# Optimization experiments

Hardware: AMD Instinct MI355X
Metric: run time of the kernel (lower is better)

## Reference

```python
import jax, jax.numpy as jnp
import numpy as np

N = 262144   # occupied voxels
H = 64       # channels
G = 128      # dense grid extent per axis (coords in [0, G))
K = 27       # 3x3x3 kernel offsets


def _build_neighbor_map():
    rng = np.random.default_rng(0)
    lin = rng.choice(G ** 3, size=N, replace=False).astype(np.int64)
    coords = np.stack(np.unravel_index(lin, (G, G, G)), axis=1)  # [N,3]
    table = np.full(G ** 3, N, dtype=np.int32)  # sentinel N -> zero row
    table[lin] = np.arange(N, dtype=np.int32)
    offs = np.array([(dx, dy, dz) for dx in (-1, 0, 1)
                     for dy in (-1, 0, 1) for dz in (-1, 0, 1)], dtype=np.int64)
    nbr = np.full((N, K), N, dtype=np.int32)
    for k in range(K):
        nc = coords + offs[k]
        ok = np.all((nc >= 0) & (nc < G), axis=1)
        nl = nc[ok, 0] * G * G + nc[ok, 1] * G + nc[ok, 2]
        nbr[ok, k] = table[nl]
    return nbr


def setup_inputs() -> dict:
    key = jax.random.key(0)
    k1, k2, k3 = jax.random.split(key, 3)
    scale = 1.0 / np.sqrt(K * H)  # ME-style fan-in init scale
    x = jax.random.normal(k1, (N, H), dtype=jnp.float32)
    Wa = jax.random.normal(k2, (K, H, H), dtype=jnp.float32) * scale
    Wb = jax.random.normal(k3, (K, H, H), dtype=jnp.float32) * scale
    nbr = jnp.asarray(_build_neighbor_map())
    return {"x": x, "Wa": Wa, "Wb": Wb, "nbr": nbr}


def _sparse_conv(feats, W, nbr):
    # gather -> GEMM -> accumulate, per kernel offset (missing neighbors hit zero row)
    fpad = jnp.concatenate([feats, jnp.zeros((1, feats.shape[1]), feats.dtype)], axis=0)
    out = jnp.zeros((feats.shape[0], W.shape[2]), feats.dtype)
    for k in range(W.shape[0]):
        out = out + fpad[nbr[:, k]] @ W[k]
    return out


def reference(x, Wa, Wb, nbr):
    out = _sparse_conv(x, Wa, nbr)          # spconva
    out = jax.nn.relu(out)                  # MinkowskiReLU
    out = _sparse_conv(out, Wb, nbr)        # spconvb
    return out + x                          # residual add
```

## Files before the change

### kernel.cpp

```cpp
#include <hip/hip_runtime.h>


#define N_ROWS 262144
#define HCH    64
#define KOFF   27
#define CHUNK  3

typedef unsigned short u16;
typedef __attribute__((ext_vector_type(8))) short short8;
typedef __attribute__((ext_vector_type(4))) float f32x4;

__device__ __forceinline__ u16 f2bf(float f) {
    unsigned u = __builtin_bit_cast(unsigned, f);
    unsigned r = (u + 0x7FFFu + ((u >> 16) & 1u)) >> 16;
    return (u16)r;
}
__device__ __forceinline__ float bf2f(u16 h) {
    return __builtin_bit_cast(float, (unsigned)h << 16);
}
__device__ __forceinline__ unsigned pack2(float a, float b) {
    return (unsigned)f2bf(a) | ((unsigned)f2bf(b) << 16);
}

__global__ void prep_all(const float* __restrict__ x, u16* __restrict__ xb,
                         u16* __restrict__ yb,
                         const float* __restrict__ Wa, const float* __restrict__ Wb,
                         u16* __restrict__ Wta, u16* __restrict__ Wtb,
                         const int* __restrict__ nbr, int* __restrict__ nbrT) {
    const int b = blockIdx.x;
    if (b < 8193) {
        long gid = (long)b * 256 + threadIdx.x;
        const long total = (long)N_ROWS * HCH / 8;
        if (gid < total) {
            const float4* s = (const float4*)(x + gid * 8);
            float4 a = s[0], c = s[1];
            uint4 v;
            v.x = pack2(a.x, a.y); v.y = pack2(a.z, a.w);
            v.z = pack2(c.x, c.y); v.w = pack2(c.z, c.w);
            *(uint4*)(xb + gid * 8) = v;
        } else if (gid < total + HCH / 8) {
            long c = gid - total;
            uint4 z; z.x = 0; z.y = 0; z.z = 0; z.w = 0;
            *(uint4*)(xb + (long)N_ROWS * HCH + c * 8) = z;
            *(uint4*)(yb + (long)N_ROWS * HCH + c * 8) = z;
        }
    } else if (b < 9057) {
        int gid = (b - 8193) * 256 + threadIdx.x;
        const int total = KOFF * HCH * HCH;
        const float* src; u16* dst; int e;
        if (gid < total)          { src = Wa; dst = Wta; e = gid; }
        else if (gid < 2 * total) { src = Wb; dst = Wtb; e = gid - total; }
        else return;
        int k = e >> 12, i = (e >> 6) & 63, j = e & 63;
        dst[(k << 12) + (j << 6) + i] = f2bf(src[e]);
    } else {
        __shared__ int t[32 * 27];
        const int rowbase = (b - 9057) * 32;
        for (int e = threadIdx.x; e < 32 * 27; e += 256)
            t[e] = nbr[(size_t)rowbase * KOFF + e];
        __syncthreads();
        for (int e = threadIdx.x; e < 32 * 27; e += 256) {
            int k = e >> 5, r = e & 31;
            nbrT[(size_t)k * N_ROWS + rowbase + r] = t[r * KOFF + k];
        }
    }
}

template <bool FIRST>
__global__ __launch_bounds__(256, 2) void conv_kernel(
    const u16* __restrict__ xg,
    const u16* __restrict__ Wt,
    const int* __restrict__ nb,
    u16* __restrict__ ybf,
    float* __restrict__ outf,
    const u16* __restrict__ residb)
{
    __shared__ uint4 Wlds4[CHUNK * 512];
    u16*   Wsh = (u16*)Wlds4;
    float* Fsh = (float*)Wlds4;

    const int tid  = threadIdx.x;
    const int wave = tid >> 6;
    const int lane = tid & 63;
    const int m    = lane & 15;
    const int q    = lane >> 4;
    const int base = blockIdx.x * 256 + wave * 64;

    int row[4];
#pragma unroll
    for (int t = 0; t < 4; t++) row[t] = base + t * 16 + m;

    auto ld_idx = [&](int k, int t) -> int {
        return nb[(size_t)k * N_ROWS + row[t]];
    };

    auto ldA = [&](int idx, short8& a0, short8& a1) {
        const u16* ar = xg + (size_t)idx * HCH + q * 8;
        a0 = *(const short8*)ar;
        a1 = *(const short8*)(ar + 32);
    };

    f32x4 acc[4][4];
#pragma unroll
    for (int t = 0; t < 4; t++)
#pragma unroll
        for (int jt = 0; jt < 4; jt++)
            acc[t][jt] = (f32x4){0.f, 0.f, 0.f, 0.f};

    int i0[4], i1[4], idxRing[2][4];
#pragma unroll
    for (int t = 0; t < 4; t++) i0[t] = ld_idx(0, t);
#pragma unroll
    for (int t = 0; t < 4; t++) i1[t] = ld_idx(1, t);
#pragma unroll
    for (int t = 0; t < 4; t++) idxRing[0][t] = ld_idx(2, t);
#pragma unroll
    for (int t = 0; t < 4; t++) idxRing[1][t] = ld_idx(3, t);

    short8 Aring[3][4][2];
#pragma unroll
    for (int t = 0; t < 4; t++) ldA(i0[t], Aring[0][t][0], Aring[0][t][1]);
#pragma unroll
    for (int t = 0; t < 4; t++) ldA(i1[t], Aring[1][t][0], Aring[1][t][1]);

#pragma unroll
    for (int c = 0; c < KOFF / CHUNK; c++) {
        __syncthreads();
        const uint4* wg = (const uint4*)(Wt + c * CHUNK * 4096);
#pragma unroll
        for (int e = tid; e < CHUNK * 512; e += 256) {
            uint4 v = wg[e];
            int s = e >> 9, rem = e & 511, j = rem >> 3, cc = rem & 7;
            Wlds4[s * 512 + j * 8 + (cc ^ (j & 7))] = v;
        }
        __syncthreads();

#pragma unroll
        for (int s = 0; s < CHUNK; s++) {
            const int kk  = c * CHUNK + s;
            const int par = kk & 1;
            const int cur = kk % 3;
            const int nxt = (kk + 2) % 3;

#pragma unroll
            for (int t = 0; t < 4; t++)
                ldA(idxRing[par][t], Aring[nxt][t][0], Aring[nxt][t][1]);
            const int k4 = (kk + 4 < KOFF) ? kk + 4 : KOFF - 1;
#pragma unroll
            for (int t = 0; t < 4; t++) idxRing[par][t] = ld_idx(k4, t);

            const u16* bs = Wsh + s * 4096;
            short8 B0[4], B1[4];
#pragma unroll
            for (int jt = 0; jt < 4; jt++) {
                int j = jt * 16 + m;
                B0[jt] = *(const short8*)(bs + j * 64 + ((q    ) ^ (m & 7)) * 8);
                B1[jt] = *(const short8*)(bs + j * 64 + ((q + 4) ^ (m & 7)) * 8);
            }

#pragma unroll
            for (int t = 0; t < 4; t++)
#pragma unroll
                for (int jt = 0; jt < 4; jt++)
                    acc[t][jt] = __builtin_amdgcn_mfma_f32_16x16x32_bf16(
                        Aring[cur][t][0], B0[jt], acc[t][jt], 0, 0, 0);
#pragma unroll
            for (int t = 0; t < 4; t++)
#pragma unroll
                for (int jt = 0; jt < 4; jt++)
                    acc[t][jt] = __builtin_amdgcn_mfma_f32_16x16x32_bf16(
                        Aring[cur][t][1], B1[jt], acc[t][jt], 0, 0, 0);
        }
    }

    float* sl = Fsh + wave * (16 * 68);
    const int r = lane & 15;
    const int h = lane >> 4;
#pragma unroll
    for (int t = 0; t < 4; t++) {
        __syncthreads();
#pragma unroll
        for (int jt = 0; jt < 4; jt++)
#pragma unroll
            for (int rr = 0; rr < 4; rr++)
                sl[(q * 4 + rr) * 68 + jt * 16 + m] = acc[t][jt][rr];
        __syncthreads();

        float4 v0 = *(const float4*)&sl[r * 68 + h * 16 + 0];
        float4 v1 = *(const float4*)&sl[r * 68 + h * 16 + 4];
        float4 v2 = *(const float4*)&sl[r * 68 + h * 16 + 8];
        float4 v3 = *(const float4*)&sl[r * 68 + h * 16 + 12];
        const size_t grow = (size_t)(base + t * 16 + r);
        if (FIRST) {
            uint4 o0, o1;
            o0.x = pack2(fmaxf(v0.x, 0.f), fmaxf(v0.y, 0.f));
            o0.y = pack2(fmaxf(v0.z, 0.f), fmaxf(v0.w, 0.f));
            o0.z = pack2(fmaxf(v1.x, 0.f), fmaxf(v1.y, 0.f));
            o0.w = pack2(fmaxf(v1.z, 0.f), fmaxf(v1.w, 0.f));
            o1.x = pack2(fmaxf(v2.x, 0.f), fmaxf(v2.y, 0.f));
            o1.y = pack2(fmaxf(v2.z, 0.f), fmaxf(v2.w, 0.f));
            o1.z = pack2(fmaxf(v3.x, 0.f), fmaxf(v3.y, 0.f));
            o1.w = pack2(fmaxf(v3.z, 0.f), fmaxf(v3.w, 0.f));
            uint4* dst = (uint4*)(ybf + grow * HCH + h * 16);
            dst[0] = o0; dst[1] = o1;
        } else {
            const uint4* rb = (const uint4*)(residb + grow * HCH + h * 16);
            uint4 r0 = rb[0], r1 = rb[1];
            float4 o;
            float* op = outf + grow * HCH + h * 16;
            o.x = v0.x + bf2f((u16)(r0.x & 0xFFFF));
            o.y = v0.y + bf2f((u16)(r0.x >> 16));
            o.z = v0.z + bf2f((u16)(r0.y & 0xFFFF));
            o.w = v0.w + bf2f((u16)(r0.y >> 16));
            *(float4*)(op + 0) = o;
            o.x = v1.x + bf2f((u16)(r0.z & 0xFFFF));
            o.y = v1.y + bf2f((u16)(r0.z >> 16));
            o.z = v1.z + bf2f((u16)(r0.w & 0xFFFF));
            o.w = v1.w + bf2f((u16)(r0.w >> 16));
            *(float4*)(op + 4) = o;
            o.x = v2.x + bf2f((u16)(r1.x & 0xFFFF));
            o.y = v2.y + bf2f((u16)(r1.x >> 16));
            o.z = v2.z + bf2f((u16)(r1.y & 0xFFFF));
            o.w = v2.w + bf2f((u16)(r1.y >> 16));
            *(float4*)(op + 8) = o;
            o.x = v3.x + bf2f((u16)(r1.z & 0xFFFF));
            o.y = v3.y + bf2f((u16)(r1.z >> 16));
            o.z = v3.z + bf2f((u16)(r1.w & 0xFFFF));
            o.w = v3.w + bf2f((u16)(r1.w >> 16));
            *(float4*)(op + 12) = o;
        }
    }
}

extern "C" void kernel_launch(void* const* d_in, const int* in_sizes, int n_in,
                              void* d_out, int out_size, void* d_ws, size_t ws_size,
                              hipStream_t stream) {
    const float* x   = (const float*)d_in[0];
    const float* Wa  = (const float*)d_in[1];
    const float* Wb  = (const float*)d_in[2];
    const int*   nbr = (const int*)d_in[3];
    float* out = (float*)d_out;

    char* ws = (char*)d_ws;
    const size_t xb_bytes = (size_t)(N_ROWS + 1) * HCH * sizeof(u16);
    const size_t w_bytes  = (size_t)KOFF * HCH * HCH * sizeof(u16);
    u16* xb  = (u16*)ws;
    u16* yb  = (u16*)(ws + xb_bytes);
    u16* Wta = (u16*)(ws + 2 * xb_bytes);
    u16* Wtb = (u16*)(ws + 2 * xb_bytes + w_bytes);
    int* nbrT = (int*)(ws + 2 * xb_bytes + 2 * w_bytes);

    prep_all<<<17249, 256, 0, stream>>>(x, xb, yb, Wa, Wb, Wta, Wtb, nbr, nbrT);
    conv_kernel<true ><<<N_ROWS / 256, 256, 0, stream>>>(xb, Wta, nbrT, yb, nullptr, nullptr);
    conv_kernel<false><<<N_ROWS / 256, 256, 0, stream>>>(yb, Wtb, nbrT, nullptr, out, xb);
}
```

Before: 312.1 us.

## Load weight fragments directly from global memory instead of staging through LDS

Removes the per-chunk cooperative copy of weight slices into shared memory and the block-wide barriers around it. Each lane now reads its B fragments straight from global (L1/L2-cached) weights every offset, and the epilogue transpose drops its __syncthreads since each wave uses a private LDS slice. This cuts barrier stalls and LDS traffic, and shrinks the shared allocation so more blocks may fit, at the cost of extra global/cache loads per wave.

```diff
diff --git a/kernel.cpp b/kernel.cpp
--- a/kernel.cpp
+++ b/kernel.cpp
@@ -4,7 +4,6 @@
 #define N_ROWS 262144
 #define HCH    64
 #define KOFF   27
-#define CHUNK  3
 
 typedef unsigned short u16;
 typedef __attribute__((ext_vector_type(8))) short short8;
@@ -75,9 +74,7 @@
     float* __restrict__ outf,
     const u16* __restrict__ residb)
 {
-    __shared__ uint4 Wlds4[CHUNK * 512];
-    u16*   Wsh = (u16*)Wlds4;
-    float* Fsh = (float*)Wlds4;
+    __shared__ float Fsh[4 * 16 * 68];
 
     const int tid  = threadIdx.x;
     const int wave = tid >> 6;
@@ -100,6 +97,8 @@
         a1 = *(const short8*)(ar + 32);
     };
 
+    const u16* bbase = Wt + m * 64 + q * 8;
+
     f32x4 acc[4][4];
 #pragma unroll
     for (int t = 0; t < 4; t++)
@@ -123,54 +122,41 @@
 #pragma unroll
     for (int t = 0; t < 4; t++) ldA(i1[t], Aring[1][t][0], Aring[1][t][1]);
 
-#pragma unroll
-    for (int c = 0; c < KOFF / CHUNK; c++) {
-        __syncthreads();
-        const uint4* wg = (const uint4*)(Wt + c * CHUNK * 4096);
-#pragma unroll
-        for (int e = tid; e < CHUNK * 512; e += 256) {
-            uint4 v = wg[e];
-            int s = e >> 9, rem = e & 511, j = rem >> 3, cc = rem & 7;
-            Wlds4[s * 512 + j * 8 + (cc ^ (j & 7))] = v;
-        }
-        __syncthreads();
-
-#pragma unroll
-        for (int s = 0; s < CHUNK; s++) {
-            const int kk  = c * CHUNK + s;
-            const int par = kk & 1;
-            const int cur = kk % 3;
-            const int nxt = (kk + 2) % 3;
-
-#pragma unroll
-            for (int t = 0; t < 4; t++)
-                ldA(idxRing[par][t], Aring[nxt][t][0], Aring[nxt][t][1]);
-            const int k4 = (kk + 4 < KOFF) ? kk + 4 : KOFF - 1;
-#pragma unroll
-            for (int t = 0; t < 4; t++) idxRing[par][t] = ld_idx(k4, t);
-
-            const u16* bs = Wsh + s * 4096;
-            short8 B0[4], B1[4];
-#pragma unroll
-            for (int jt = 0; jt < 4; jt++) {
-                int j = jt * 16 + m;
-                B0[jt] = *(const short8*)(bs + j * 64 + ((q    ) ^ (m & 7)) * 8);
-                B1[jt] = *(const short8*)(bs + j * 64 + ((q + 4) ^ (m & 7)) * 8);
-            }
-
-#pragma unroll
-            for (int t = 0; t < 4; t++)
-#pragma unroll
-                for (int jt = 0; jt < 4; jt++)
-                    acc[t][jt] = __builtin_amdgcn_mfma_f32_16x16x32_bf16(
-                        Aring[cur][t][0], B0[jt], acc[t][jt], 0, 0, 0);
-#pragma unroll
-            for (int t = 0; t < 4; t++)
-#pragma unroll
-                for (int jt = 0; jt < 4; jt++)
-                    acc[t][jt] = __builtin_amdgcn_mfma_f32_16x16x32_bf16(
-                        Aring[cur][t][1], B1[jt], acc[t][jt], 0, 0, 0);
-        }
+#pragma unroll 3
+    for (int kk = 0; kk < KOFF; kk++) {
+        const int par = kk & 1;
+        const int cur = kk % 3;
+        const int nxt = (kk + 2) % 3;
+        const u16* bs = bbase + kk * 4096;
+
+        short8 B0[4], B1[4];
+#pragma unroll
+        for (int jt = 0; jt < 4; jt++)
+            B0[jt] = *(const short8*)(bs + jt * 1024);
+
+#pragma unroll
+        for (int t = 0; t < 4; t++)
+            ldA(idxRing[par][t], Aring[nxt][t][0], Aring[nxt][t][1]);
+        const int k4 = (kk + 4 < KOFF) ? kk + 4 : KOFF - 1;
+#pragma unroll
+        for (int t = 0; t < 4; t++) idxRing[par][t] = ld_idx(k4, t);
+
+#pragma unroll
+        for (int jt = 0; jt < 4; jt++)
+            B1[jt] = *(const short8*)(bs + jt * 1024 + 32);
+
+#pragma unroll
+        for (int t = 0; t < 4; t++)
+#pragma unroll
+            for (int jt = 0; jt < 4; jt++)
+                acc[t][jt] = __builtin_amdgcn_mfma_f32_16x16x32_bf16(
+                    Aring[cur][t][0], B0[jt], acc[t][jt], 0, 0, 0);
+#pragma unroll
+        for (int t = 0; t < 4; t++)
+#pragma unroll
+            for (int jt = 0; jt < 4; jt++)
+                acc[t][jt] = __builtin_amdgcn_mfma_f32_16x16x32_bf16(
+                    Aring[cur][t][1], B1[jt], acc[t][jt], 0, 0, 0);
     }
 
     float* sl = Fsh + wave * (16 * 68);
@@ -178,13 +164,11 @@
     const int h = lane >> 4;
 #pragma unroll
     for (int t = 0; t < 4; t++) {
-        __syncthreads();
 #pragma unroll
         for (int jt = 0; jt < 4; jt++)
 #pragma unroll
             for (int rr = 0; rr < 4; rr++)
                 sl[(q * 4 + rr) * 68 + jt * 16 + m] = acc[t][jt][rr];
-        __syncthreads();
 
         float4 v0 = *(const float4*)&sl[r * 68 + h * 16 + 0];
         float4 v1 = *(const float4*)&sl[r * 68 + h * 16 + 4];
```

Result: slower. 459.1 us (+47.1%).
